# Kernel tuning notes

Measured on AMD Instinct MI355X. Metric: run time of the kernel, lower is better.

Reference implementation:

```python
import jax, jax.numpy as jnp
import numpy as np

# quantization / activation scales (stand-ins for act_scales dict entries)
S_IN = 0.05      # in_proj:input
S_Z = 0.02       # in_proj:output (also gate/z scale)
S_U = 0.01       # x_proj:input (conv output scale)
S_DTLN = 0.02    # dt_layernorm:output
S_B = 0.02       # B_layernorm:output
S_C = 0.02       # C_layernorm:output
S_DT = 0.01      # dt_proj:output
S_Y = 0.01       # out_proj:input
EPS = 1e-6
R = 128          # time_step_rank
N = 16           # ssm_state_size


def qa(x, s):
    # simulate int8 activation quantization (values kept in fp32)
    return jnp.clip(jnp.round(x / s), -128.0, 127.0)


def qw(w):
    # per-tensor symmetric int8 weight quantization
    s = jnp.max(jnp.abs(w)) / 127.0
    return jnp.clip(jnp.round(w / s), -128.0, 127.0), s


def rmsnorm_q(x, w, s):
    x = x.astype(jnp.float32)
    x = x * jax.lax.rsqrt(jnp.mean(x * x, axis=-1, keepdims=True) + EPS)
    return qa(w * x, s)


def ssm_scan(u, dt, A, Bm, Cm):
    # u, dt: [B, D, S]; Bm, Cm: [B, S, N]; A: [D, N]
    def step(h, xs):
        dt_t, u_t, B_t, C_t = xs                     # [B,D],[B,D],[B,N],[B,N]
        dA = jnp.exp(dt_t[..., None] * A)            # [B,D,N]
        h = h * dA + (dt_t * u_t)[..., None] * B_t[:, None, :]
        y = jnp.einsum('bdn,bn->bd', h, C_t)
        return h, y
    Bsz, Dd, S = u.shape
    h0 = jnp.zeros((Bsz, Dd, A.shape[1]), u.dtype)
    xs = (jnp.moveaxis(dt, 2, 0), jnp.moveaxis(u, 2, 0),
          jnp.moveaxis(Bm, 1, 0), jnp.moveaxis(Cm, 1, 0))
    _, ys = jax.lax.scan(step, h0, xs)               # ys: [S,B,D]
    return jnp.moveaxis(ys, 0, 2)                    # [B,D,S]


def setup_inputs() -> dict:
    key = jax.random.key(0)
    ks = jax.random.split(key, 10)
    B, S, H, Din, K = 2, 2048, 2048, 4096, 4
    return {
        'hidden_states': jax.random.normal(ks[0], (B, S, H), jnp.float32),
        'in_proj_w': jax.random.normal(ks[1], (2 * Din, H), jnp.float32) * 0.02,
        'conv_w': jax.random.normal(ks[2], (Din, K), jnp.float32) * 0.1,
        'conv_b': jax.random.normal(ks[3], (Din,), jnp.float32) * 0.01,
        'x_proj_w': jax.random.normal(ks[4], (R + 2 * N, Din), jnp.float32) * 0.02,
        'dt_ln_w': jnp.ones((R,), jnp.float32),
        'B_ln_w': jnp.ones((N,), jnp.float32),
        'C_ln_w': jnp.ones((N,), jnp.float32),
        'dt_proj_w': jax.random.normal(ks[5], (Din, R), jnp.float32) * 0.05,
        'dt_bias': jax.random.normal(ks[6], (Din,), jnp.float32) * 0.5 - 4.0,
        'A_log': jnp.log(jnp.broadcast_to(jnp.arange(1, N + 1, dtype=jnp.float32), (Din, N))),
        'D_skip': jnp.ones((Din,), jnp.float32),
        'out_proj_w': jax.random.normal(ks[7], (H, Din), jnp.float32) * 0.02,
    }


def reference(hidden_states, in_proj_w, conv_w, conv_b, x_proj_w, dt_ln_w,
              B_ln_w, C_ln_w, dt_proj_w, dt_bias, A_log, D_skip, out_proj_w):
    # --- in_proj (W8A8B8O8), then seqlen-last layout [B, 2D, S] ---
    x_q = qa(hidden_states, S_IN)
    wq, ws = qw(in_proj_w)
    proj_q = qa((x_q @ wq.T) * (S_IN * ws), S_Z)          # [B,S,2D] int8-valued
    proj_q = jnp.swapaxes(proj_q, 1, 2)                   # [B,2D,S]
    Din = proj_q.shape[1] // 2
    hs_q, gate_q = proj_q[:, :Din], proj_q[:, Din:]

    # --- quantized causal depthwise conv1d + silu (QCausalConv1D) ---
    cwq, cws = qw(conv_w)
    K = conv_w.shape[1]
    conv_out = jax.lax.conv_general_dilated(
        hs_q, cwq[:, None, :], (1,), [(K - 1, 0)],
        dimension_numbers=('NCH', 'OIH', 'NCH'), feature_group_count=Din)
    conv_out = conv_out * (S_Z * cws) + conv_b[None, :, None]
    u_q = qa(jax.nn.silu(conv_out), S_U)                  # [B,Din,S]

    # --- x_proj (W8A8BF16OF16) -> dt/B/C, inner RMSNorms + quant ---
    xwq, xws = qw(x_proj_w)
    ssm_p = (jnp.swapaxes(u_q, 1, 2) @ xwq.T) * (S_U * xws)   # [B,S,R+2N] float
    dt_q = rmsnorm_q(ssm_p[..., :R], dt_ln_w, S_DTLN)
    B_q = rmsnorm_q(ssm_p[..., R:R + N], B_ln_w, S_B)
    C_q = rmsnorm_q(ssm_p[..., R + N:], C_ln_w, S_C)

    # --- dt_proj (W8A8B8O8, bias folded into scan) ---
    dwq, dws = qw(dt_proj_w)
    dt8 = qa((dt_q @ dwq.T) * (S_DTLN * dws), S_DT)       # [B,S,Din]
    dt = jax.nn.softplus(jnp.swapaxes(dt8, 1, 2) * S_DT + dt_bias[None, :, None])

    # --- selective scan (QSScan): dequantize, recur, gate ---
    u = u_q * S_U
    A = -jnp.exp(A_log)
    ys = ssm_scan(u, dt, A, B_q * S_B, C_q * S_C)         # [B,Din,S]
    ys = ys + u * D_skip[None, :, None]
    ys = ys * jax.nn.silu(gate_q * S_Z)

    # --- QAct + out_proj (W8A8BF16OF16) ---
    y_q = qa(jnp.swapaxes(ys, 1, 2), S_Y)                 # [B,S,Din]
    owq, ows = qw(out_proj_w)
    return (y_q @ owq.T) * (S_Y * ows)                    # [B,S,H]
```

## Files before the change

kernel.cpp:

```cpp
#include <hip/hip_runtime.h>
#include <stdint.h>

typedef signed char i8;
typedef int v4i __attribute__((ext_vector_type(4)));

#define S_IN  0.05f
#define S_Z   0.02f
#define S_U   0.01f
#define S_DTLN 0.02f
#define S_B   0.02f
#define S_C   0.02f
#define S_DT  0.01f
#define S_Y   0.01f

__device__ __forceinline__ float q8f(float x, float s) {
    float r = rintf(x / s);
    return fmaxf(-128.0f, fminf(127.0f, r));
}
__device__ __forceinline__ int q8i(float x, float s) { return (int)q8f(x, s); }

__device__ __forceinline__ float softplus_f(float x) {
    return __fadd_rn(fmaxf(x, 0.0f), log1pf(expf(-fabsf(x))));
}

__device__ __forceinline__ int sbyte_of(int w, int j) {
    return (int)(signed char)((unsigned)w >> (j * 8));
}

__device__ __forceinline__ void gload16(const i8* g, i8* lds) {
    __builtin_amdgcn_global_load_lds(
        (const __attribute__((address_space(1))) unsigned int*)g,
        (__attribute__((address_space(3))) unsigned int*)lds,
        16, 0, 0);
}

__global__ __launch_bounds__(256)
void k_maxabs(const float* __restrict__ w, long long n, unsigned* __restrict__ out) {
    unsigned m = 0;
    long long stride = (long long)gridDim.x * 256;
    for (long long i = (long long)blockIdx.x * 256 + threadIdx.x; i < n; i += stride)
        m = max(m, __float_as_uint(fabsf(w[i])));
    #pragma unroll
    for (int off = 32; off; off >>= 1) {
        unsigned o = (unsigned)__shfl_xor((int)m, off);
        m = max(m, o);
    }
    __shared__ unsigned sm[4];
    if ((threadIdx.x & 63) == 0) sm[threadIdx.x >> 6] = m;
    __syncthreads();
    if (threadIdx.x == 0) {
        unsigned r = max(max(sm[0], sm[1]), max(sm[2], sm[3]));
        atomicMax(out, r);
    }
}

__global__ __launch_bounds__(256)
void k_quant_w(const float* __restrict__ w, long long n,
               const unsigned* __restrict__ maxbits, i8* __restrict__ o) {
    long long i = ((long long)blockIdx.x * 256 + threadIdx.x) * 4;
    if (i >= n) return;
    float s = __uint_as_float(*maxbits) / 127.0f;
    float4 v = *(const float4*)(w + i);
    unsigned pk = ((unsigned)(q8i(v.x, s) & 255))
                | ((unsigned)(q8i(v.y, s) & 255) << 8)
                | ((unsigned)(q8i(v.z, s) & 255) << 16)
                | ((unsigned)(q8i(v.w, s) & 255) << 24);
    *(unsigned*)(o + i) = pk;
}

__global__ __launch_bounds__(256)
void k_quant_x(const float* __restrict__ x, long long n, float s, i8* __restrict__ o) {
    long long i = ((long long)blockIdx.x * 256 + threadIdx.x) * 4;
    if (i >= n) return;
    float4 v = *(const float4*)(x + i);
    unsigned pk = ((unsigned)(q8i(v.x, s) & 255))
                | ((unsigned)(q8i(v.y, s) & 255) << 8)
                | ((unsigned)(q8i(v.z, s) & 255) << 16)
                | ((unsigned)(q8i(v.w, s) & 255) << 24);
    *(unsigned*)(o + i) = pk;
}

template<int EPI>
__global__ __launch_bounds__(256)
void k_mgemm(const i8* __restrict__ A, const i8* __restrict__ Bw,
             int M, int N, int K,
             const unsigned* __restrict__ wmaxbits,
             void* __restrict__ out0, void* __restrict__ out1) {
    __shared__ i8 sA[8192];
    __shared__ i8 sB[8192];
    const int tid = threadIdx.x;
    const int w = tid >> 6;
    const int l = tid & 63;
    const int m0 = blockIdx.y << 7;
    const int n0 = blockIdx.x << 7;
    const int lr = l & 15;
    const int lk = l >> 4;
    const i8* gA0 = A  + (size_t)(m0 + (w * 16) + lr) * K + lk * 16;
    const i8* gA1 = A  + (size_t)(m0 + ((4 + w) * 16) + lr) * K + lk * 16;
    const i8* gB0 = Bw + (size_t)(n0 + (w * 16) + lr) * K + lk * 16;
    const i8* gB1 = Bw + (size_t)(n0 + ((4 + w) * 16) + lr) * K + lk * 16;
    i8* lA0 = sA + (w * 1024);
    i8* lA1 = sA + ((4 + w) * 1024);
    i8* lB0 = sB + (w * 1024);
    i8* lB1 = sB + ((4 + w) * 1024);
    const int mw = (w >> 1) * 4;
    const int nw = (w & 1) * 4;
    const int rdoff = lk * 256 + lr * 16;
    v4i acc[4][4] = {};
    for (int k0 = 0; k0 < K; k0 += 64) {
        gload16(gA0 + k0, lA0);
        gload16(gA1 + k0, lA1);
        gload16(gB0 + k0, lB0);
        gload16(gB1 + k0, lB1);
        __syncthreads();
        v4i af[4], bf[4];
        #pragma unroll
        for (int t = 0; t < 4; t++) {
            af[t] = *(const v4i*)(sA + (mw + t) * 1024 + rdoff);
            bf[t] = *(const v4i*)(sB + (nw + t) * 1024 + rdoff);
        }
        #pragma unroll
        for (int mt = 0; mt < 4; mt++)
            #pragma unroll
            for (int nt = 0; nt < 4; nt++)
                acc[mt][nt] = __builtin_amdgcn_mfma_i32_16x16x64_i8(af[mt], bf[nt], acc[mt][nt], 0, 0, 0);
        __syncthreads();
    }
    const float wsc = __uint_as_float(*wmaxbits) / 127.0f;
    const int m0w = m0 + (w >> 1) * 64;
    const int n0w = n0 + (w & 1) * 64;
    if constexpr (EPI == 0 || EPI == 2) {
        const float sc = (EPI == 0 ? S_IN : S_DTLN) * wsc;
        const float qs = (EPI == 0 ? S_Z : S_DT);
        const int b = m0w >> 11;
        #pragma unroll
        for (int nt = 0; nt < 4; nt++) {
            const int j = n0w + nt * 16 + lr;
            i8* dst;
            if constexpr (EPI == 0) dst = (j < 4096) ? (i8*)out0 : (i8*)out1;
            else dst = (i8*)out0;
            const int jj = j & 4095;
            #pragma unroll
            for (int mt = 0; mt < 4; mt++) {
                const int sbase = (m0w & 2047) + mt * 16 + lk * 4;
                unsigned pk = 0;
                #pragma unroll
                for (int r = 0; r < 4; r++) {
                    float v = (float)acc[mt][nt][r] * sc;
                    pk |= ((unsigned)(q8i(v, qs) & 255)) << (8 * r);
                }
                *(unsigned*)(dst + ((size_t)b * 4096 + jj) * 2048 + sbase) = pk;
            }
        }
    } else if constexpr (EPI == 1) {
        const float sc = S_U * wsc;
        float* O = (float*)out0;
        #pragma unroll
        for (int mt = 0; mt < 4; mt++)
            #pragma unroll
            for (int r = 0; r < 4; r++) {
                const int m = m0w + mt * 16 + lk * 4 + r;
                #pragma unroll
                for (int nt = 0; nt < 4; nt++) {
                    const int j = n0w + nt * 16 + lr;
                    if (j < 160)
                        O[(size_t)m * 160 + j] = (float)acc[mt][nt][r] * sc;
                }
            }
    } else {
        const float sc = S_Y * wsc;
        float* O = (float*)out0;
        #pragma unroll
        for (int mt = 0; mt < 4; mt++)
            #pragma unroll
            for (int r = 0; r < 4; r++) {
                const int m = m0w + mt * 16 + lk * 4 + r;
                #pragma unroll
                for (int nt = 0; nt < 4; nt++)
                    O[(size_t)m * N + n0w + nt * 16 + lr] = (float)acc[mt][nt][r] * sc;
            }
    }
}

__global__ __launch_bounds__(256)
void k_conv(const i8* __restrict__ hsq, const i8* __restrict__ cwq,
            const float* __restrict__ conv_b, const unsigned* __restrict__ cmaxbits,
            i8* __restrict__ uq, i8* __restrict__ uqT) {
    __shared__ char lt[64][68];
    const int tid = threadIdx.x;
    const int b = blockIdx.z;
    const int d0 = blockIdx.y << 6;
    const int s0 = blockIdx.x << 6;
    const int dl = tid >> 2;
    const int sg = tid & 3;
    const int d = d0 + dl;
    const int sbase = s0 + (sg << 4);
    const i8* xp = hsq + ((size_t)b * 4096 + d) * 2048;
    int v[19];
    #pragma unroll
    for (int i = 0; i < 19; i++) {
        int s = sbase - 3 + i;
        v[i] = (s >= 0) ? (int)xp[s] : 0;
    }
    const unsigned cw = *(const unsigned*)(cwq + (size_t)d * 4);
    const int w0 = (int)(char)(cw & 255);
    const int w1 = (int)(char)((cw >> 8) & 255);
    const int w2 = (int)(char)((cw >> 16) & 255);
    const int w3 = (int)(char)((cw >> 24) & 255);
    const float cws = __uint_as_float(*cmaxbits) / 127.0f;
    const float sc = S_Z * cws;
    const float bias = conv_b[d];
    unsigned pk[4] = {0, 0, 0, 0};
    #pragma unroll
    for (int t = 0; t < 16; t++) {
        int acc = v[t] * w0 + v[t + 1] * w1 + v[t + 2] * w2 + v[t + 3] * w3;
        float f = __fadd_rn(__fmul_rn((float)acc, sc), bias);
        float sig = 1.0f / (1.0f + expf(-f));
        float sl = __fmul_rn(f, sig);
        int q = q8i(sl, S_U);
        pk[t >> 2] |= ((unsigned)(q & 255)) << ((t & 3) * 8);
        lt[(sg << 4) + t][dl] = (char)q;
    }
    *(int4*)(uq + ((size_t)b * 4096 + d) * 2048 + sbase) = make_int4(pk[0], pk[1], pk[2], pk[3]);
    __syncthreads();
    const int rr = tid >> 2;
    const int wg = tid & 3;
    const int* rp = (const int*)(&lt[rr][wg << 4]);
    int4 o; o.x = rp[0]; o.y = rp[1]; o.z = rp[2]; o.w = rp[3];
    *(int4*)(uqT + ((size_t)b * 2048 + s0 + rr) * 4096 + d0 + (wg << 4)) = o;
}

__global__ __launch_bounds__(64)
void k_rms(const float* __restrict__ p,
           const float* __restrict__ wdt, const float* __restrict__ wB, const float* __restrict__ wC,
           i8* __restrict__ dtq, i8* __restrict__ bqT, i8* __restrict__ cqT) {
    const int row = blockIdx.x;
    const int lane = threadIdx.x;
    const float* x = p + (size_t)row * 160;
    float a0 = x[lane], a1 = x[64 + lane];
    float bb = (lane < 16) ? x[128 + lane] : 0.0f;
    float cc = (lane < 16) ? x[144 + lane] : 0.0f;
    float sdt = __fadd_rn(__fmul_rn(a0, a0), __fmul_rn(a1, a1));
    float sB = __fmul_rn(bb, bb);
    float sC = __fmul_rn(cc, cc);
    #pragma unroll
    for (int off = 32; off; off >>= 1) {
        sdt = __fadd_rn(sdt, __shfl_xor(sdt, off));
        sB  = __fadd_rn(sB,  __shfl_xor(sB, off));
        sC  = __fadd_rn(sC,  __shfl_xor(sC, off));
    }
    float rdt = 1.0f / sqrtf(sdt / 128.0f + 1e-6f);
    float rB  = 1.0f / sqrtf(sB / 16.0f + 1e-6f);
    float rC  = 1.0f / sqrtf(sC / 16.0f + 1e-6f);
    dtq[(size_t)row * 128 + lane]      = (i8)q8i(__fmul_rn(wdt[lane],      __fmul_rn(a0, rdt)), S_DTLN);
    dtq[(size_t)row * 128 + 64 + lane] = (i8)q8i(__fmul_rn(wdt[64 + lane], __fmul_rn(a1, rdt)), S_DTLN);
    if (lane < 16) {
        size_t tpos = ((size_t)(row >> 11) * 16 + lane) * 2048 + (row & 2047);
        bqT[tpos] = (i8)q8i(__fmul_rn(wB[lane], __fmul_rn(bb, rB)), S_B);
        cqT[tpos] = (i8)q8i(__fmul_rn(wC[lane], __fmul_rn(cc, rC)), S_C);
    }
}

__global__ __launch_bounds__(256)
void k_lut_dt(const float* __restrict__ dt_bias, float* __restrict__ lut) {
    const int d = blockIdx.x;
    const int q = threadIdx.x;
    const float bias = dt_bias[d];
    lut[(size_t)d * 256 + q] =
        softplus_f(__fadd_rn(__fmul_rn((float)(q - 128), S_DT), bias));
}
__global__ __launch_bounds__(256)
void k_lut_silu(float* __restrict__ lut) {
    const int q = threadIdx.x;
    float gv = __fmul_rn((float)(q - 128), S_Z);
    float sg = __fmul_rn(gv, 1.0f / (1.0f + expf(-gv)));
    lut[q] = sg;
}

__global__ __launch_bounds__(256)
void k_scan4(const i8* __restrict__ dt8, const i8* __restrict__ uq, const i8* __restrict__ gq,
             const i8* __restrict__ BqT, const i8* __restrict__ CqT,
             const float* __restrict__ lut_dt, const float* __restrict__ lut_silu,
             const float* __restrict__ A_log, const float* __restrict__ D_skip,
             i8* __restrict__ yq) {
    const int g = blockIdx.x * 256 + threadIdx.x;
    const int n = g & 15;
    const int bd = g >> 4;
    const int d = bd & 4095;
    const int b = bd >> 12;
    const float Acoef = -expf(A_log[(size_t)d * 16 + n]);
    const float Dd = D_skip[d];
    const float* ldt = lut_dt + (size_t)d * 256;
    const v4i* dtp = (const v4i*)(dt8 + (size_t)bd * 2048);
    const v4i* up  = (const v4i*)(uq  + (size_t)bd * 2048);
    const v4i* gp  = (const v4i*)(gq  + (size_t)bd * 2048);
    const v4i* Bp  = (const v4i*)(BqT + ((size_t)b * 16 + n) * 2048);
    const v4i* Cp  = (const v4i*)(CqT + ((size_t)b * 16 + n) * 2048);
    i8* yp = yq + (size_t)b * 2048 * 4096 + d;
    float h = 0.0f;
    v4i dtw = dtp[0], uw = up[0], gw = gp[0], bw = Bp[0], cw = Cp[0];
    for (int t = 0; t < 128; t++) {
        v4i ndt, nu, ng, nb, nc;
        if (t < 127) { ndt = dtp[t + 1]; nu = up[t + 1]; ng = gp[t + 1]; nb = Bp[t + 1]; nc = Cp[t + 1]; }
        float dtv[16], dA[16], pj[16], Cv[16], y[16];
        #pragma unroll
        for (int j = 0; j < 16; j++)
            dtv[j] = ldt[sbyte_of(dtw[j >> 2], j & 3) + 128];
        #pragma unroll
        for (int j = 0; j < 16; j++)
            dA[j] = expf(__fmul_rn(dtv[j], Acoef));
        #pragma unroll
        for (int j = 0; j < 16; j++) {
            float uv = __fmul_rn((float)sbyte_of(uw[j >> 2], j & 3), S_U);
            float Bv = __fmul_rn((float)sbyte_of(bw[j >> 2], j & 3), S_B);
            Cv[j] = __fmul_rn((float)sbyte_of(cw[j >> 2], j & 3), S_C);
            pj[j] = __fmul_rn(__fmul_rn(dtv[j], uv), Bv);
        }
        #pragma unroll
        for (int j = 0; j < 16; j++) {
            h = __fadd_rn(__fmul_rn(h, dA[j]), pj[j]);
            y[j] = __fmul_rn(h, Cv[j]);
        }
        float w8[8];
        #pragma unroll
        for (int i = 0; i < 8; i++) {
            float a = y[2 * i], bq = y[2 * i + 1];
            float snd = (n & 1) ? a : bq;
            float rcv = __shfl_xor(snd, 1);
            float kept = (n & 1) ? bq : a;
            w8[i] = __fadd_rn(kept, rcv);
        }
        float w4[4];
        #pragma unroll
        for (int i = 0; i < 4; i++) {
            float a = w8[2 * i], bq = w8[2 * i + 1];
            float snd = (n & 2) ? a : bq;
            float rcv = __shfl_xor(snd, 2);
            float kept = (n & 2) ? bq : a;
            w4[i] = __fadd_rn(kept, rcv);
        }
        float w2[2];
        #pragma unroll
        for (int i = 0; i < 2; i++) {
            float a = w4[2 * i], bq = w4[2 * i + 1];
            float snd = (n & 4) ? a : bq;
            float rcv = __shfl_xor(snd, 4);
            float kept = (n & 4) ? bq : a;
            w2[i] = __fadd_rn(kept, rcv);
        }
        float ysave;
        {
            float a = w2[0], bq = w2[1];
            float snd = (n & 8) ? a : bq;
            float rcv = __shfl_xor(snd, 8);
            float kept = (n & 8) ? bq : a;
            ysave = __fadd_rn(kept, rcv);
        }
        int uws = (n & 8) ? ((n & 4) ? uw[3] : uw[2]) : ((n & 4) ? uw[1] : uw[0]);
        int gws = (n & 8) ? ((n & 4) ? gw[3] : gw[2]) : ((n & 4) ? gw[1] : gw[0]);
        float uvn = __fmul_rn((float)(int)(signed char)((unsigned)uws >> ((n & 3) * 8)), S_U);
        int gb = (int)(signed char)((unsigned)gws >> ((n & 3) * 8));
        float ys = __fadd_rn(ysave, __fmul_rn(uvn, Dd));
        float sg = lut_silu[gb + 128];
        float vv = __fmul_rn(ys, sg);
        yp[(size_t)(t * 16 + n) * 4096] = (i8)q8i(vv, S_Y);
        if (t < 127) { dtw = ndt; uw = nu; gw = ng; bw = nb; cw = nc; }
    }
}

extern "C" void kernel_launch(void* const* d_in, const int* in_sizes, int n_in,
                              void* d_out, int out_size, void* d_ws, size_t ws_size,
                              hipStream_t stream) {
    const float* hidden   = (const float*)d_in[0];
    const float* in_proj  = (const float*)d_in[1];
    const float* conv_w   = (const float*)d_in[2];
    const float* conv_b   = (const float*)d_in[3];
    const float* x_proj   = (const float*)d_in[4];
    const float* dt_ln    = (const float*)d_in[5];
    const float* B_ln     = (const float*)d_in[6];
    const float* C_ln     = (const float*)d_in[7];
    const float* dt_proj  = (const float*)d_in[8];
    const float* dt_bias  = (const float*)d_in[9];
    const float* A_log    = (const float*)d_in[10];
    const float* D_skip   = (const float*)d_in[11];
    const float* out_proj = (const float*)d_in[12];
    float* out = (float*)d_out;

    char* ws = (char*)d_ws;
    unsigned* scales = (unsigned*)ws;
    i8* WQ   = (i8*)(ws + 256);
    i8* XQ   = (i8*)(ws + 16777472);
    i8* HSQ  = (i8*)(ws + 25166080);
    char* S0 = ws + 41943296;
    float* SSMP = (float*)S0;
    i8* XWQp = (i8*)(S0 + 2621440);
    i8* DTQb = (i8*)(S0 + 3670016);
    i8* DWQ  = (i8*)(S0 + 4194304);
    i8* CWQ  = (i8*)(S0 + 4718592);
    float* LUTSI = (float*)(S0 + 4734976);
    i8* BQT  = (i8*)(S0 + 4736000);
    i8* CQT  = (i8*)(S0 + 4801536);
    float* LUTDT = (float*)S0;

    i8* GQ = (i8*)d_out;
    i8* UQ = (i8*)d_out + 16777216;
    i8* UQT = WQ;
    i8* OWQ = XQ;
    i8* DT8 = HSQ;
    i8* YQ  = WQ;

    hipMemsetAsync(scales, 0, 256, stream);
    hipMemsetAsync(XWQp, 0, 1048576, stream);

    k_maxabs<<<2048, 256, 0, stream>>>(in_proj, 16777216LL, scales + 0);
    k_maxabs<<<64,   256, 0, stream>>>(conv_w,  16384LL,    scales + 1);
    k_maxabs<<<512,  256, 0, stream>>>(x_proj,  655360LL,   scales + 2);
    k_maxabs<<<512,  256, 0, stream>>>(dt_proj, 524288LL,   scales + 3);
    k_maxabs<<<1024, 256, 0, stream>>>(out_proj, 8388608LL, scales + 4);

    k_quant_w<<<16384, 256, 0, stream>>>(in_proj, 16777216LL, scales + 0, WQ);
    k_quant_w<<<16,    256, 0, stream>>>(conv_w,  16384LL,    scales + 1, CWQ);
    k_quant_w<<<640,   256, 0, stream>>>(x_proj,  655360LL,   scales + 2, XWQp);
    k_quant_w<<<512,   256, 0, stream>>>(dt_proj, 524288LL,   scales + 3, DWQ);
    k_quant_x<<<8192,  256, 0, stream>>>(hidden,  8388608LL,  S_IN, XQ);

    k_mgemm<0><<<dim3(64, 32), 256, 0, stream>>>(XQ, WQ, 4096, 8192, 2048, scales + 0, HSQ, GQ);

    k_quant_w<<<8192, 256, 0, stream>>>(out_proj, 8388608LL, scales + 4, OWQ);

    dim3 gc(32, 64, 2);
    k_conv<<<gc, 256, 0, stream>>>(HSQ, CWQ, conv_b, scales + 1, UQ, UQT);

    k_mgemm<1><<<dim3(2, 32), 256, 0, stream>>>(UQT, XWQp, 4096, 256, 4096, scales + 2, SSMP, nullptr);

    k_rms<<<4096, 64, 0, stream>>>(SSMP, dt_ln, B_ln, C_ln, DTQb, BQT, CQT);

    k_mgemm<2><<<dim3(32, 32), 256, 0, stream>>>(DTQb, DWQ, 4096, 4096, 128, scales + 3, DT8, nullptr);

    k_lut_dt<<<4096, 256, 0, stream>>>(dt_bias, LUTDT);
    k_lut_silu<<<1, 256, 0, stream>>>(LUTSI);

    k_scan4<<<512, 256, 0, stream>>>(DT8, UQ, GQ, BQT, CQT, LUTDT, LUTSI, A_log, D_skip, YQ);

    k_mgemm<3><<<dim3(16, 32), 256, 0, stream>>>(YQ, OWQ, 4096, 2048, 4096, scales + 4, out, nullptr);
}
```

Measured before the change: 717.9 us.

## Deepen int8 GEMM K-tile, swizzle block order, index LUTs by unsigned byte

The int8 MFMA GEMM now stages 128 K-elements per iteration instead of 64, which doubles LDS use and halves the number of barrier pairs per tile. Block IDs are remapped so consecutive blocks are spread in groups of eight, aiming at better L2 or cache locality across the grid. The dt and silu lookup tables are re-indexed by the raw unsigned byte, which removes a sign extension and add in the scan's inner loop. The larger LDS footprint may reduce occupancy, and the remap assumes the grid size divides evenly by eight.

```diff
diff --git a/kernel.cpp b/kernel.cpp
--- a/kernel.cpp
+++ b/kernel.cpp
@@ -25,6 +25,9 @@
 
 __device__ __forceinline__ int sbyte_of(int w, int j) {
     return (int)(signed char)((unsigned)w >> (j * 8));
+}
+__device__ __forceinline__ int ubyte_of(int w, int j) {
+    return (int)(((unsigned)w >> (j * 8)) & 255u);
 }
 
 __device__ __forceinline__ void gload16(const i8* g, i8* lds) {
@@ -86,44 +89,49 @@
              int M, int N, int K,
              const unsigned* __restrict__ wmaxbits,
              void* __restrict__ out0, void* __restrict__ out1) {
-    __shared__ i8 sA[8192];
-    __shared__ i8 sB[8192];
+    __shared__ i8 sA[16384];
+    __shared__ i8 sB[16384];
     const int tid = threadIdx.x;
     const int w = tid >> 6;
     const int l = tid & 63;
-    const int m0 = blockIdx.y << 7;
-    const int n0 = blockIdx.x << 7;
+    int id = blockIdx.y * gridDim.x + blockIdx.x;
+    const int qq = (gridDim.x * gridDim.y) >> 3;
+    id = (id & 7) * qq + (id >> 3);
+    const int m0 = (id / gridDim.x) << 7;
+    const int n0 = (id % gridDim.x) << 7;
     const int lr = l & 15;
     const int lk = l >> 4;
-    const i8* gA0 = A  + (size_t)(m0 + (w * 16) + lr) * K + lk * 16;
-    const i8* gA1 = A  + (size_t)(m0 + ((4 + w) * 16) + lr) * K + lk * 16;
-    const i8* gB0 = Bw + (size_t)(n0 + (w * 16) + lr) * K + lk * 16;
-    const i8* gB1 = Bw + (size_t)(n0 + ((4 + w) * 16) + lr) * K + lk * 16;
-    i8* lA0 = sA + (w * 1024);
-    i8* lA1 = sA + ((4 + w) * 1024);
-    i8* lB0 = sB + (w * 1024);
-    i8* lB1 = sB + ((4 + w) * 1024);
+    const i8* gA = A  + (size_t)(m0 + lr) * K + lk * 16;
+    const i8* gB = Bw + (size_t)(n0 + lr) * K + lk * 16;
+    const size_t rowK16 = (size_t)16 * K;
     const int mw = (w >> 1) * 4;
     const int nw = (w & 1) * 4;
     const int rdoff = lk * 256 + lr * 16;
     v4i acc[4][4] = {};
-    for (int k0 = 0; k0 < K; k0 += 64) {
-        gload16(gA0 + k0, lA0);
-        gload16(gA1 + k0, lA1);
-        gload16(gB0 + k0, lB0);
-        gload16(gB1 + k0, lB1);
+    for (int k0 = 0; k0 < K; k0 += 128) {
+        gload16(gA + rowK16 * w + k0,            sA + w * 2048);
+        gload16(gA + rowK16 * w + k0 + 64,       sA + w * 2048 + 1024);
+        gload16(gA + rowK16 * (4 + w) + k0,      sA + (4 + w) * 2048);
+        gload16(gA + rowK16 * (4 + w) + k0 + 64, sA + (4 + w) * 2048 + 1024);
+        gload16(gB + rowK16 * w + k0,            sB + w * 2048);
+        gload16(gB + rowK16 * w + k0 + 64,       sB + w * 2048 + 1024);
+        gload16(gB + rowK16 * (4 + w) + k0,      sB + (4 + w) * 2048);
+        gload16(gB + rowK16 * (4 + w) + k0 + 64, sB + (4 + w) * 2048 + 1024);
         __syncthreads();
-        v4i af[4], bf[4];
-        #pragma unroll
-        for (int t = 0; t < 4; t++) {
-            af[t] = *(const v4i*)(sA + (mw + t) * 1024 + rdoff);
-            bf[t] = *(const v4i*)(sB + (nw + t) * 1024 + rdoff);
-        }
-        #pragma unroll
-        for (int mt = 0; mt < 4; mt++)
+        #pragma unroll
+        for (int k64 = 0; k64 < 2; k64++) {
+            v4i af[4], bf[4];
             #pragma unroll
-            for (int nt = 0; nt < 4; nt++)
-                acc[mt][nt] = __builtin_amdgcn_mfma_i32_16x16x64_i8(af[mt], bf[nt], acc[mt][nt], 0, 0, 0);
+            for (int t = 0; t < 4; t++) {
+                af[t] = *(const v4i*)(sA + (mw + t) * 2048 + k64 * 1024 + rdoff);
+                bf[t] = *(const v4i*)(sB + (nw + t) * 2048 + k64 * 1024 + rdoff);
+            }
+            #pragma unroll
+            for (int mt = 0; mt < 4; mt++)
+                #pragma unroll
+                for (int nt = 0; nt < 4; nt++)
+                    acc[mt][nt] = __builtin_amdgcn_mfma_i32_16x16x64_i8(af[mt], bf[nt], acc[mt][nt], 0, 0, 0);
+        }
         __syncthreads();
     }
     const float wsc = __uint_as_float(*wmaxbits) / 127.0f;
@@ -265,14 +273,16 @@
 void k_lut_dt(const float* __restrict__ dt_bias, float* __restrict__ lut) {
     const int d = blockIdx.x;
     const int q = threadIdx.x;
+    const int sv = (q < 128) ? q : q - 256;
     const float bias = dt_bias[d];
     lut[(size_t)d * 256 + q] =
-        softplus_f(__fadd_rn(__fmul_rn((float)(q - 128), S_DT), bias));
+        softplus_f(__fadd_rn(__fmul_rn((float)sv, S_DT), bias));
 }
 __global__ __launch_bounds__(256)
 void k_lut_silu(float* __restrict__ lut) {
     const int q = threadIdx.x;
-    float gv = __fmul_rn((float)(q - 128), S_Z);
+    const int sv = (q < 128) ? q : q - 256;
+    float gv = __fmul_rn((float)sv, S_Z);
     float sg = __fmul_rn(gv, 1.0f / (1.0f + expf(-gv)));
     lut[q] = sg;
 }
@@ -305,7 +315,7 @@
         float dtv[16], dA[16], pj[16], Cv[16], y[16];
         #pragma unroll
         for (int j = 0; j < 16; j++)
-            dtv[j] = ldt[sbyte_of(dtw[j >> 2], j & 3) + 128];
+            dtv[j] = ldt[ubyte_of(dtw[j >> 2], j & 3)];
         #pragma unroll
         for (int j = 0; j < 16; j++)
             dA[j] = expf(__fmul_rn(dtv[j], Acoef));
@@ -359,9 +369,9 @@
         int uws = (n & 8) ? ((n & 4) ? uw[3] : uw[2]) : ((n & 4) ? uw[1] : uw[0]);
         int gws = (n & 8) ? ((n & 4) ? gw[3] : gw[2]) : ((n & 4) ? gw[1] : gw[0]);
         float uvn = __fmul_rn((float)(int)(signed char)((unsigned)uws >> ((n & 3) * 8)), S_U);
-        int gb = (int)(signed char)((unsigned)gws >> ((n & 3) * 8));
+        int gb = (int)(((unsigned)gws >> ((n & 3) * 8)) & 255u);
         float ys = __fadd_rn(ysave, __fmul_rn(uvn, Dd));
-        float sg = lut_silu[gb + 128];
+        float sg = lut_silu[gb];
         float vv = __fmul_rn(ys, sg);
         yp[(size_t)(t * 16 + n) * 4096] = (i8)q8i(vv, S_Y);
         if (t < 127) { dtw = ndt; uw = nu; gw = ng; bw = nb; cw = nc; }
```

Result: faster. 702.0 us (-2.2%).
